# Performance work log

Measured on AMD Instinct MI355X. Metric: run time of the kernel, lower is better.

The kernel has to match this reference:

```python
import jax, jax.numpy as jnp
import numpy as np

N_NODES = 50000
N_EDGES = 300000
N_GRAPHS = 2048
N_FEATS = 128
DIM_OUT = 32


def setup_inputs() -> dict:
    key = jax.random.key(0)
    ks = jax.random.split(key, 10)
    def glorot(k, shape):
        fan_in, fan_out = shape
        lim = (6.0 / (fan_in + fan_out)) ** 0.5
        return jax.random.uniform(k, shape, jnp.float32, -lim, lim)
    x = jax.random.normal(ks[0], (N_NODES, N_FEATS), jnp.float32)
    edge_index = jax.random.randint(ks[1], (2, N_EDGES), 0, N_NODES, jnp.int64)
    batch = jnp.sort(jax.random.randint(ks[2], (N_NODES,), 0, N_GRAPHS, jnp.int64))
    return {
        "x": x,
        "edge_index": edge_index,
        "batch": batch,
        "W1": glorot(ks[3], (N_FEATS, 256)), "b1": jnp.zeros((256,), jnp.float32),
        "W2": glorot(ks[4], (256, 256)),     "b2": jnp.zeros((256,), jnp.float32),
        "W3": glorot(ks[5], (256, 256)),     "b3": jnp.zeros((256,), jnp.float32),
        "Wf1": glorot(ks[6], (256, 128)),    "bf1": jnp.zeros((128,), jnp.float32),
        "Wf2": glorot(ks[7], (128, DIM_OUT)), "bf2": jnp.zeros((DIM_OUT,), jnp.float32),
    }


def _gcn_norm(edge_index, num_nodes):
    # PyG GCNConv default: add self-loops, symmetric D^-1/2 (A+I) D^-1/2 norm.
    loop = jnp.arange(num_nodes, dtype=edge_index.dtype)
    src = jnp.concatenate([edge_index[0], loop])
    dst = jnp.concatenate([edge_index[1], loop])
    deg = jax.ops.segment_sum(jnp.ones_like(dst, jnp.float32), dst, num_segments=num_nodes)
    dinv = jnp.where(deg > 0, deg ** -0.5, 0.0)
    norm = dinv[src] * dinv[dst]  # [E + N]
    return src, dst, norm


def _gcn_conv(x, src, dst, norm, W, b):
    h = x @ W                                # [N, C] transform first (efficient)
    msg = h[src] * norm[:, None]             # gather + scale, [E+N, C]
    agg = jax.ops.segment_sum(msg, dst, num_segments=x.shape[0])
    return agg + b


def reference(x, edge_index, batch, W1, b1, W2, b2, W3, b3, Wf1, bf1, Wf2, bf2):
    n = x.shape[0]
    src, dst, norm = _gcn_norm(edge_index, n)
    h = jax.nn.relu(_gcn_conv(x, src, dst, norm, W1, b1))
    h = jax.nn.relu(_gcn_conv(h, src, dst, norm, W2, b2))
    h = jax.nn.relu(_gcn_conv(h, src, dst, norm, W3, b3))
    # global_mean_pool over batch segment ids
    sums = jax.ops.segment_sum(h, batch, num_segments=N_GRAPHS)
    cnts = jax.ops.segment_sum(jnp.ones((n,), jnp.float32), batch, num_segments=N_GRAPHS)
    hg = sums / jnp.maximum(cnts, 1.0)[:, None]
    h = jax.nn.relu(hg @ Wf1 + bf1)
    return h @ Wf2 + bf2  # [N_GRAPHS, DIM_OUT]
```

## Files before the change

kernel.cpp:

```cpp
#include <hip/hip_runtime.h>
#include <hip/hip_bf16.h>

#define NNODES 50000
#define NEDGES 300000
#define NGRAPH 2048
#define NFEAT  128
#define NHID   256
#define DOUT   32
#define NROWS  50048

typedef __bf16 bf16x8 __attribute__((ext_vector_type(8)));
typedef float  f32x4  __attribute__((ext_vector_type(4)));
typedef unsigned short ushort8v __attribute__((ext_vector_type(8)));
typedef __attribute__((address_space(1))) const void* gas_ptr;
typedef __attribute__((address_space(3))) void* las_ptr;

__device__ __forceinline__ float bf2f(unsigned short u) {
    return __uint_as_float(((unsigned)u) << 16);
}
__device__ __forceinline__ unsigned short f2bf(float f) {
    unsigned u = __float_as_uint(f);
    unsigned r = u + 0x7FFFu + ((u >> 16) & 1u);
    return (unsigned short)(r >> 16);
}


__global__ __launch_bounds__(256) void prep_k(const float* __restrict__ x, unsigned short* __restrict__ x16,
                                              const float* __restrict__ W1, const float* __restrict__ W2,
                                              const float* __restrict__ W3, const float* __restrict__ Wf1,
                                              const float* __restrict__ Wf2,
                                              unsigned short* __restrict__ Wt1, unsigned short* __restrict__ Wt2,
                                              unsigned short* __restrict__ Wt3, unsigned short* __restrict__ Wf1t,
                                              unsigned short* __restrict__ Wf2t,
                                              int* __restrict__ cnt, int* __restrict__ fill,
                                              int4* __restrict__ adj8z) {
    int idx = blockIdx.x * 256 + threadIdx.x;
    if (idx < 800000) {
        int i = idx * 8;
        float4 a = *(const float4*)&x[i];
        float4 b = *(const float4*)&x[i + 4];
        ushort8v o = { f2bf(a.x), f2bf(a.y), f2bf(a.z), f2bf(a.w),
                       f2bf(b.x), f2bf(b.y), f2bf(b.z), f2bf(b.w) };
        int row = idx >> 4, ch = idx & 15;
        ((ushort8v*)x16)[(size_t)(row << 4) | (ch ^ (row & 7))] = o;
        return;
    }
    int t = idx - 800000;
    if (t < 200704) {
        const float* W; unsigned short* Wt; int K, N, base; bool sw;
        if      (t <  32768) { W = W1;  Wt = Wt1;  K = 128; N = 256; base = 0;      sw = true; }
        else if (t <  98304) { W = W2;  Wt = Wt2;  K = 256; N = 256; base = 32768;  sw = true; }
        else if (t < 163840) { W = W3;  Wt = Wt3;  K = 256; N = 256; base = 98304;  sw = true; }
        else if (t < 196608) { W = Wf1; Wt = Wf1t; K = 256; N = 128; base = 163840; sw = false; }
        else                 { W = Wf2; Wt = Wf2t; K = 128; N = 32;  base = 196608; sw = false; }
        int i = t - base; int n = i / K, k = i - n * K;
        unsigned short v = f2bf(W[(size_t)k * N + n]);
        if (sw) Wt[(k >> 5) * 8192 + n * 32 + (k & 31)] = v;
        else    Wt[i] = v;
        return;
    }
    t -= 200704;
    if (t < NNODES) { cnt[t] = 0; fill[t] = 0; return; }
    t -= NNODES;
    if (t < 200000) { int4 z4 = {0, 0, 0, 0}; adj8z[t] = z4; }
}

__global__ __launch_bounds__(256) void edge_hist_k(const int* __restrict__ dst, int* cnt, int E) {
    int e = blockIdx.x * 256 + threadIdx.x;
    if (e < E) atomicAdd(&cnt[dst[e]], 1);
}

__global__ __launch_bounds__(1024) void scan_block_k(const int* __restrict__ cnt, int* __restrict__ rowp,
                                                     int* __restrict__ part, float* __restrict__ dinv,
                                                     int2* __restrict__ hdr, int n) {
    __shared__ int s[1024];
    int tid = threadIdx.x;
    int i = blockIdx.x * 1024 + tid;
    int v = (i < n) ? cnt[i] : 0;
    if (i < n) {
        float dv = rsqrtf((float)(v + 1));
        dinv[i] = dv;
        hdr[i] = make_int2(v, __float_as_int(dv * dv));
    }
    s[tid] = v;
    __syncthreads();
    for (int off = 1; off < 1024; off <<= 1) {
        int t = (tid >= off) ? s[tid - off] : 0;
        __syncthreads();
        s[tid] += t;
        __syncthreads();
    }
    if (i < n) rowp[i] = s[tid] - v;
    if (tid == 1023) part[blockIdx.x] = s[1023];
}

__global__ __launch_bounds__(256) void scatter_k(const int* __restrict__ src, const int* __restrict__ dst,
                                                 const int* __restrict__ rowp_pre, const int* __restrict__ part,
                                                 int* fill, const float* __restrict__ dinv,
                                                 int2* __restrict__ adj8, int2* __restrict__ adj,
                                                 int* __restrict__ rowp_fin,
                                                 const int* __restrict__ batch, int* __restrict__ gstart,
                                                 int E, int n, int nb) {
    __shared__ int s[64];
    int tid = threadIdx.x;
    if (tid < 64) s[tid] = (tid < nb) ? part[tid] : 0;
    __syncthreads();
    for (int off = 1; off < 64; off <<= 1) {
        int t = 0;
        if (tid < 64 && tid >= off) t = s[tid - off];
        __syncthreads();
        if (tid < 64) s[tid] += t;
        __syncthreads();
    }
    int gid = blockIdx.x * 256 + tid;
    if (gid <= n) {
        if (gid < n) {
            int ch = gid >> 10;
            int base = (ch == 0) ? 0 : s[ch - 1];
            rowp_fin[gid] = rowp_pre[gid] + base;
        } else {
            rowp_fin[n] = s[nb - 1];
        }
    }
    if (gid < n) {
        int b = batch[gid];
        int prev = (gid == 0) ? -1 : batch[gid - 1];
        for (int g = prev + 1; g <= b; ++g) gstart[g] = gid;
        if (gid == n - 1)
            for (int g = b + 1; g <= NGRAPH; ++g) gstart[g] = n;
    }
    if (gid < E) {
        int ss = src[gid], d = dst[gid];
        int f = atomicAdd(&fill[d], 1);
        int2 a; a.x = ss; a.y = __float_as_int(dinv[ss] * dinv[d]);
        if (f < 8) {
            adj8[d * 8 + f] = a;
        } else {
            int ch = d >> 10;
            int base = (ch == 0) ? 0 : s[ch - 1];
            adj[rowp_pre[d] + base + f] = a;
        }
    }
}

template<int CH>
__global__ __launch_bounds__(256) void agg_k(const unsigned short* __restrict__ T,
                                             const int4* __restrict__ adj8,
                                             const int2* __restrict__ hdr,
                                             const int* __restrict__ rowf,
                                             const int2* __restrict__ adj,
                                             unsigned short* __restrict__ z, int n) {
    int g  = threadIdx.x / CH;
    int li = threadIdx.x % CH;
    int node = blockIdx.x * (256 / CH) + g;
    if (node >= n) return;
    const ushort8v* tp = (const ushort8v*)T;
    int2 h = hdr[node];
    int deg = h.x;
    float sw = __int_as_float(h.y);
    ushort8v u = tp[(size_t)node * CH + (li ^ (node & 7))];
    int4 s4[4];
#pragma unroll
    for (int j = 0; j < 4; ++j) s4[j] = adj8[node * 4 + j];
    float ac[8];
#pragma unroll
    for (int k = 0; k < 8; ++k) ac[k] = bf2f(u[k]) * sw;
    int c[8]; float w[8];
#pragma unroll
    for (int j = 0; j < 4; ++j) {
        c[2 * j]     = s4[j].x; w[2 * j]     = __int_as_float(s4[j].y);
        c[2 * j + 1] = s4[j].z; w[2 * j + 1] = __int_as_float(s4[j].w);
    }
    ushort8v mm[8];
#pragma unroll
    for (int j = 0; j < 8; ++j) mm[j] = tp[(size_t)c[j] * CH + (li ^ (c[j] & 7))];
#pragma unroll
    for (int j = 0; j < 8; ++j)
#pragma unroll
        for (int k = 0; k < 8; ++k)
            ac[k] += bf2f(mm[j][k]) * w[j];
    if (deg > 8) {
        int e0 = rowf[node], e1 = e0 + deg;
        for (int e = e0 + 8; e < e1; e += 4) {
            int2 a2[4];
#pragma unroll
            for (int j = 0; j < 4; ++j) {
                int ee = e + j;
                a2[j] = (ee < e1) ? adj[ee] : make_int2(0, 0);
            }
            ushort8v m2[4];
#pragma unroll
            for (int j = 0; j < 4; ++j) m2[j] = tp[(size_t)a2[j].x * CH + (li ^ (a2[j].x & 7))];
#pragma unroll
            for (int j = 0; j < 4; ++j)
#pragma unroll
                for (int k = 0; k < 8; ++k)
                    ac[k] += bf2f(m2[j][k]) * __int_as_float(a2[j].y);
        }
    }
    ushort8v o;
#pragma unroll
    for (int k = 0; k < 8; ++k) o[k] = f2bf(ac[k]);
    ((ushort8v*)z)[(size_t)node * CH + (li ^ (node & 7))] = o;
}

template<int K>
__global__ __launch_bounds__(512, 2) void gemm_k(const unsigned short* __restrict__ A,
                                                 const unsigned short* __restrict__ Bsw,
                                                 const float* __restrict__ bias,
                                                 unsigned short* __restrict__ C,
                                                 int M, int flags, int ntiles) {
    constexpr int CPR = K / 8;
    constexpr int LP  = (64 * CPR) / 512;
    __shared__ unsigned short At[64 * K];
    __shared__ unsigned short Et[64 * 264];
    const int tid = threadIdx.x;
    const int lane = tid & 63;
    const int wave = tid >> 6;
    const int m = lane & 15, q = lane >> 4;
    const int wr = (wave >> 2) * 32;
    const int wc = (wave & 3) * 64;

    bf16x8 breg[K / 32][4];
#pragma unroll
    for (int kt = 0; kt < K / 32; ++kt)
#pragma unroll
        for (int j = 0; j < 4; ++j)
            breg[kt][j] = *(const bf16x8*)&Bsw[kt * 8192 + (wc + j * 16 + m) * 32 + q * 8];

    for (int t = blockIdx.x; t < ntiles; t += gridDim.x) {
        const size_t cbase = (size_t)t * 64 * CPR;
#pragma unroll
        for (int p = 0; p < LP; ++p) {
            int u = p * 512 + tid;
            __builtin_amdgcn_global_load_lds((gas_ptr)(A + (cbase + u) * 8),
                                             (las_ptr)&At[(p * 512 + wave * 64) * 8], 16, 0, 0);
        }
        __syncthreads();

        f32x4 acc[2][4] = {};
#pragma unroll
        for (int kt = 0; kt < K / 32; ++kt) {
            bf16x8 af[2];
#pragma unroll
            for (int i = 0; i < 2; ++i) {
                int lr = wr + i * 16 + m;
                af[i] = *(const bf16x8*)&At[(lr * CPR + ((kt * 4 + q) ^ (lr & 7))) * 8];
            }
#pragma unroll
            for (int i = 0; i < 2; ++i)
#pragma unroll
                for (int j = 0; j < 4; ++j)
                    acc[i][j] = __builtin_amdgcn_mfma_f32_16x16x32_bf16(af[i], breg[kt][j], acc[i][j], 0, 0, 0);
        }

#pragma unroll
        for (int i = 0; i < 2; ++i) {
#pragma unroll
            for (int j = 0; j < 4; ++j) {
                int c = wc + j * 16 + m;
                float bv = (flags & 2) ? bias[c] : 0.f;
#pragma unroll
                for (int r = 0; r < 4; ++r) {
                    float v = acc[i][j][r] + bv;
                    if (flags & 1) v = fmaxf(v, 0.f);
                    Et[(wr + i * 16 + q * 4 + r) * 264 + c] = f2bf(v);
                }
            }
        }
        __syncthreads();
#pragma unroll
        for (int u0 = 0; u0 < 4; ++u0) {
            int u = u0 * 512 + tid;
            int row = u >> 5, cc = u & 31;
            int rr = t * 64 + row;
            if (rr < M)
                ((ushort8v*)C)[(size_t)rr * 32 + (cc ^ (rr & 7))] = *(const ushort8v*)&Et[row * 264 + cc * 8];
        }
    }
}

__global__ __launch_bounds__(256) void pool_k(const unsigned short* __restrict__ h,
                                              const int* __restrict__ gstart,
                                              unsigned short* __restrict__ hg) {
    __shared__ float red[4][256];
    int g = blockIdx.x;
    int wave = threadIdx.x >> 6, lane = threadIdx.x & 63;
    int s = gstart[g], e = gstart[g + 1];
    int ch = lane >> 1, sub = lane & 1;
    const ushort4* hp = (const ushort4*)h;
    float4 acc = make_float4(0.f, 0.f, 0.f, 0.f);
    for (int i = s + wave; i < e; i += 4) {
        ushort4 v = hp[((size_t)i * 32 + (ch ^ (i & 7))) * 2 + sub];
        acc.x += bf2f(v.x); acc.y += bf2f(v.y); acc.z += bf2f(v.z); acc.w += bf2f(v.w);
    }
    *(float4*)&red[wave][lane * 4] = acc;
    __syncthreads();
    if (wave == 0) {
        float inv = 1.f / fmaxf((float)(e - s), 1.f);
        float v0 = red[0][lane*4+0] + red[1][lane*4+0] + red[2][lane*4+0] + red[3][lane*4+0];
        float v1 = red[0][lane*4+1] + red[1][lane*4+1] + red[2][lane*4+1] + red[3][lane*4+1];
        float v2 = red[0][lane*4+2] + red[1][lane*4+2] + red[2][lane*4+2] + red[3][lane*4+2];
        float v3 = red[0][lane*4+3] + red[1][lane*4+3] + red[2][lane*4+3] + red[3][lane*4+3];
        ushort4 o = { f2bf(v0 * inv), f2bf(v1 * inv), f2bf(v2 * inv), f2bf(v3 * inv) };
        ((ushort4*)(hg + (size_t)g * NHID))[lane] = o;
    }
}

__global__ __launch_bounds__(256) void mlp_head_k(const unsigned short* __restrict__ HG,
                                                  const unsigned short* __restrict__ Wf1t,
                                                  const unsigned short* __restrict__ Wf2t,
                                                  const float* __restrict__ bf1, const float* __restrict__ bf2,
                                                  float* __restrict__ out) {
    __shared__ unsigned short As1[128 * 32];
    __shared__ unsigned short Bs1[128 * 32];
    __shared__ unsigned short R[128 * 128];
    __shared__ unsigned short Bs2[32 * 128];
    const int tid = threadIdx.x;
    const int lane = tid & 63, wave = tid >> 6;
    const int m = lane & 15, q = lane >> 4;
    const int rowBase = blockIdx.x * 128;
    const int wr = (wave >> 1) * 64;
    const int wc = (wave & 1) * 64;

#pragma unroll
    for (int c2 = 0; c2 < 2; ++c2) {
        const unsigned short* g = &Wf2t[(c2 * 256 + tid) * 8];
        __builtin_amdgcn_global_load_lds((gas_ptr)g, (las_ptr)&Bs2[(c2 * 256 + wave * 64) * 8], 16, 0, 0);
    }

    f32x4 acc[4][4] = {};
    for (int kt = 0; kt < 256; kt += 32) {
#pragma unroll
        for (int c2 = 0; c2 < 2; ++c2) {
            int u = c2 * 256 + tid;
            int row = u >> 2, kp = u & 3;
            const unsigned short* ga = &HG[(size_t)(rowBase + row) * 256 + kt + kp * 8];
            const unsigned short* gb = &Wf1t[(size_t)row * 256 + kt + kp * 8];
            __builtin_amdgcn_global_load_lds((gas_ptr)ga, (las_ptr)&As1[(c2 * 256 + wave * 64) * 8], 16, 0, 0);
            __builtin_amdgcn_global_load_lds((gas_ptr)gb, (las_ptr)&Bs1[(c2 * 256 + wave * 64) * 8], 16, 0, 0);
        }
        __syncthreads();
        bf16x8 af[4], bfr[4];
#pragma unroll
        for (int i = 0; i < 4; ++i) af[i] = *(const bf16x8*)&As1[(wr + i * 16 + m) * 32 + q * 8];
#pragma unroll
        for (int j = 0; j < 4; ++j) bfr[j] = *(const bf16x8*)&Bs1[(wc + j * 16 + m) * 32 + q * 8];
#pragma unroll
        for (int i = 0; i < 4; ++i)
#pragma unroll
            for (int j = 0; j < 4; ++j)
                acc[i][j] = __builtin_amdgcn_mfma_f32_16x16x32_bf16(af[i], bfr[j], acc[i][j], 0, 0, 0);
        __syncthreads();
    }
#pragma unroll
    for (int i = 0; i < 4; ++i)
#pragma unroll
        for (int j = 0; j < 4; ++j) {
            int c = wc + j * 16 + m;
            float bv = bf1[c];
#pragma unroll
            for (int r = 0; r < 4; ++r) {
                int rr = wr + i * 16 + q * 4 + r;
                R[rr * 128 + c] = f2bf(fmaxf(acc[i][j][r] + bv, 0.f));
            }
        }
    __syncthreads();

    const int wr2 = wave * 32;
    f32x4 acc2[2][2] = {};
#pragma unroll
    for (int s2 = 0; s2 < 4; ++s2) {
        bf16x8 af2[2], bf22[2];
#pragma unroll
        for (int i = 0; i < 2; ++i) af2[i] = *(const bf16x8*)&R[(wr2 + i * 16 + m) * 128 + s2 * 32 + q * 8];
#pragma unroll
        for (int ct = 0; ct < 2; ++ct) bf22[ct] = *(const bf16x8*)&Bs2[(ct * 16 + m) * 128 + s2 * 32 + q * 8];
#pragma unroll
        for (int i = 0; i < 2; ++i)
#pragma unroll
            for (int ct = 0; ct < 2; ++ct)
                acc2[i][ct] = __builtin_amdgcn_mfma_f32_16x16x32_bf16(af2[i], bf22[ct], acc2[i][ct], 0, 0, 0);
    }
#pragma unroll
    for (int i = 0; i < 2; ++i)
#pragma unroll
        for (int ct = 0; ct < 2; ++ct) {
            int c = ct * 16 + m;
            float bv = bf2[c];
#pragma unroll
            for (int r = 0; r < 4; ++r) {
                int rr = rowBase + wr2 + i * 16 + q * 4 + r;
                out[(size_t)rr * 32 + c] = acc2[i][ct][r] + bv;
            }
        }
}

extern "C" void kernel_launch(void* const* d_in, const int* in_sizes, int n_in,
                              void* d_out, int out_size, void* d_ws, size_t ws_size,
                              hipStream_t stream) {
    const float* x    = (const float*)d_in[0];
    const int*   ei   = (const int*)d_in[1];
    const int*   batch= (const int*)d_in[2];
    const float* W1   = (const float*)d_in[3];
    const float* b1   = (const float*)d_in[4];
    const float* W2   = (const float*)d_in[5];
    const float* b2   = (const float*)d_in[6];
    const float* W3   = (const float*)d_in[7];
    const float* b3   = (const float*)d_in[8];
    const float* Wf1  = (const float*)d_in[9];
    const float* bf1  = (const float*)d_in[10];
    const float* Wf2  = (const float*)d_in[11];
    const float* bf2  = (const float*)d_in[12];
    float* out = (float*)d_out;

    const int* e_src = ei;
    const int* e_dst = ei + NEDGES;

    char* ws = (char*)d_ws;
    size_t off = 0;
    auto alloc = [&](size_t bytes) -> void* {
        void* p = (void*)(ws + off);
        off += (bytes + 255) & ~(size_t)255;
        return p;
    };
    unsigned short* X16 = (unsigned short*)alloc((size_t)NROWS * NFEAT * 2);
    unsigned short* Za  = (unsigned short*)alloc((size_t)NROWS * NFEAT * 2);
    unsigned short* Ha  = (unsigned short*)alloc((size_t)NROWS * NHID * 2);
    unsigned short* Zb  = (unsigned short*)alloc((size_t)NROWS * NHID * 2);
    unsigned short* Wt1 = (unsigned short*)alloc((size_t)NHID * NFEAT * 2);
    unsigned short* Wt2 = (unsigned short*)alloc((size_t)NHID * NHID * 2);
    unsigned short* Wt3 = (unsigned short*)alloc((size_t)NHID * NHID * 2);
    unsigned short* Wf1t= (unsigned short*)alloc((size_t)NFEAT * NHID * 2);
    unsigned short* Wf2t= (unsigned short*)alloc((size_t)DOUT * NFEAT * 2);
    unsigned short* HG  = (unsigned short*)alloc((size_t)NGRAPH * NHID * 2);
    float* dinv = (float*)alloc((size_t)NNODES * 4);
    int*   cnt  = (int*)alloc((size_t)NNODES * 4);
    int*   fill = (int*)alloc((size_t)NNODES * 4);
    int*   rowp = (int*)alloc((size_t)(NNODES + 1) * 4);
    int*   rowf = (int*)alloc((size_t)(NNODES + 1) * 4);
    int2*  adj8 = (int2*)alloc((size_t)NNODES * 8 * 8);
    int2*  adj  = (int2*)alloc((size_t)NEDGES * 8);
    int2*  hdr  = (int2*)alloc((size_t)NNODES * 8);
    int*   part = (int*)alloc((size_t)64 * 4);
    int*   gstart = (int*)alloc((size_t)(NGRAPH + 1) * 4);
    (void)alloc(131072);

    const int nb = (NNODES + 1023) / 1024;

    hipLaunchKernelGGL(prep_k, dim3((1250704 + 255) / 256), dim3(256), 0, stream,
                       x, X16, W1, W2, W3, Wf1, Wf2, Wt1, Wt2, Wt3, Wf1t, Wf2t, cnt, fill,
                       (int4*)adj8);
    hipLaunchKernelGGL(edge_hist_k, dim3((NEDGES + 255) / 256), dim3(256), 0, stream, e_dst, cnt, NEDGES);
    hipLaunchKernelGGL(scan_block_k, dim3(nb), dim3(1024), 0, stream, cnt, rowp, part, dinv, hdr, NNODES);
    hipLaunchKernelGGL(scatter_k, dim3((NEDGES + 255) / 256), dim3(256), 0, stream,
                       e_src, e_dst, rowp, part, fill, dinv, adj8, adj, rowf, batch, gstart,
                       NEDGES, NNODES, nb);

    const int ntiles = NROWS / 64;
    hipLaunchKernelGGL((agg_k<16>), dim3((NNODES + 15) / 16), dim3(256), 0, stream,
                       X16, (const int4*)adj8, hdr, rowf, adj, Za, NNODES);
    hipLaunchKernelGGL((gemm_k<128>), dim3(512), dim3(512), 0, stream,
                       Za, Wt1, b1, Ha, NNODES, 3, ntiles);
    hipLaunchKernelGGL((agg_k<32>), dim3((NNODES + 7) / 8), dim3(256), 0, stream,
                       Ha, (const int4*)adj8, hdr, rowf, adj, Zb, NNODES);
    hipLaunchKernelGGL((gemm_k<256>), dim3(512), dim3(512), 0, stream,
                       Zb, Wt2, b2, Ha, NNODES, 3, ntiles);
    hipLaunchKernelGGL((agg_k<32>), dim3((NNODES + 7) / 8), dim3(256), 0, stream,
                       Ha, (const int4*)adj8, hdr, rowf, adj, Zb, NNODES);
    hipLaunchKernelGGL((gemm_k<256>), dim3(512), dim3(512), 0, stream,
                       Zb, Wt3, b3, Ha, NNODES, 3, ntiles);

    hipLaunchKernelGGL(pool_k, dim3(NGRAPH), dim3(256), 0, stream, Ha, gstart, HG);

    hipLaunchKernelGGL(mlp_head_k, dim3(NGRAPH / 128), dim3(256), 0, stream,
                       HG, Wf1t, Wf2t, bf1, bf2, out);
}
```

Before: 280.2 us.

## Quantize hidden activations to int8 with per-row scales for aggregation gathers

The first two GEMMs now emit int8 activations with a per-row absmax scale instead of bf16. A new aggregation kernel gathers these int8 rows, dequantizes with the row scales and accumulates in fp32. The aim is to halve the bytes moved by the bandwidth-bound neighbor gathers. It adds quantization error beyond bf16 and extra epilogue work for the reduction and packing.

```diff
diff --git a/kernel.cpp b/kernel.cpp
--- a/kernel.cpp
+++ b/kernel.cpp
@@ -22,6 +22,9 @@
     unsigned u = __float_as_uint(f);
     unsigned r = u + 0x7FFFu + ((u >> 16) & 1u);
     return (unsigned short)(r >> 16);
+}
+__device__ __forceinline__ float sb2f(unsigned v, int k) {
+    return (float)((signed char)(v >> (8 * k)));
 }
 
 
@@ -204,11 +207,86 @@
     ((ushort8v*)z)[(size_t)node * CH + (li ^ (node & 7))] = o;
 }
 
-template<int K>
+__global__ __launch_bounds__(256) void agg_q_k(const unsigned char* __restrict__ Hq,
+                                               const float* __restrict__ csc,
+                                               const int4* __restrict__ adj8,
+                                               const int2* __restrict__ hdr,
+                                               const int* __restrict__ rowf,
+                                               const int2* __restrict__ adj,
+                                               unsigned short* __restrict__ z, int n) {
+    int g  = threadIdx.x >> 5;
+    int li = threadIdx.x & 31;
+    int node = blockIdx.x * 8 + g;
+    if (node >= n) return;
+    const uint2* qp = (const uint2*)Hq;
+    int2 h = hdr[node];
+    int deg = h.x;
+    float swgt = __int_as_float(h.y) * csc[node];
+    uint2 u = qp[(size_t)node * 32 + li];
+    int4 s4[4];
+#pragma unroll
+    for (int j = 0; j < 4; ++j) s4[j] = adj8[node * 4 + j];
+    int c[8]; float w[8];
+#pragma unroll
+    for (int j = 0; j < 4; ++j) {
+        c[2 * j]     = s4[j].x; w[2 * j]     = __int_as_float(s4[j].y);
+        c[2 * j + 1] = s4[j].z; w[2 * j + 1] = __int_as_float(s4[j].w);
+    }
+    uint2 mm[8];
+#pragma unroll
+    for (int j = 0; j < 8; ++j) mm[j] = qp[(size_t)c[j] * 32 + li];
+    float ws[8];
+#pragma unroll
+    for (int j = 0; j < 8; ++j) ws[j] = w[j] * csc[c[j]];
+    float ac[8];
+#pragma unroll
+    for (int k = 0; k < 4; ++k) {
+        ac[k]     = sb2f(u.x, k) * swgt;
+        ac[k + 4] = sb2f(u.y, k) * swgt;
+    }
+#pragma unroll
+    for (int j = 0; j < 8; ++j)
+#pragma unroll
+        for (int k = 0; k < 4; ++k) {
+            ac[k]     += sb2f(mm[j].x, k) * ws[j];
+            ac[k + 4] += sb2f(mm[j].y, k) * ws[j];
+        }
+    if (deg > 8) {
+        int e0 = rowf[node], e1 = e0 + deg;
+        for (int e = e0 + 8; e < e1; e += 4) {
+            int2 a2[4];
+#pragma unroll
+            for (int j = 0; j < 4; ++j) {
+                int ee = e + j;
+                a2[j] = (ee < e1) ? adj[ee] : make_int2(0, 0);
+            }
+            uint2 m2[4]; float w2[4];
+#pragma unroll
+            for (int j = 0; j < 4; ++j) m2[j] = qp[(size_t)a2[j].x * 32 + li];
+#pragma unroll
+            for (int j = 0; j < 4; ++j) w2[j] = __int_as_float(a2[j].y) * csc[a2[j].x];
+#pragma unroll
+            for (int j = 0; j < 4; ++j)
+#pragma unroll
+                for (int k = 0; k < 4; ++k) {
+                    ac[k]     += sb2f(m2[j].x, k) * w2[j];
+                    ac[k + 4] += sb2f(m2[j].y, k) * w2[j];
+                }
+        }
+    }
+    ushort8v o;
+#pragma unroll
+    for (int k = 0; k < 8; ++k) o[k] = f2bf(ac[k]);
+    ((ushort8v*)z)[(size_t)node * 32 + (li ^ (node & 7))] = o;
+}
+
+template<int K, bool QOUT>
 __global__ __launch_bounds__(512, 2) void gemm_k(const unsigned short* __restrict__ A,
                                                  const unsigned short* __restrict__ Bsw,
                                                  const float* __restrict__ bias,
                                                  unsigned short* __restrict__ C,
+                                                 unsigned char* __restrict__ Cq,
+                                                 float* __restrict__ csc,
                                                  int M, int flags, int ntiles) {
     constexpr int CPR = K / 8;
     constexpr int LP  = (64 * CPR) / 512;
@@ -269,13 +347,51 @@
             }
         }
         __syncthreads();
-#pragma unroll
-        for (int u0 = 0; u0 < 4; ++u0) {
-            int u = u0 * 512 + tid;
-            int row = u >> 5, cc = u & 31;
+
+        if (QOUT) {
+            int row = tid >> 3, ch8 = tid & 7;
             int rr = t * 64 + row;
-            if (rr < M)
-                ((ushort8v*)C)[(size_t)rr * 32 + (cc ^ (rr & 7))] = *(const ushort8v*)&Et[row * 264 + cc * 8];
+            ushort8v e[4];
+#pragma unroll
+            for (int k2 = 0; k2 < 4; ++k2)
+                e[k2] = *(const ushort8v*)&Et[row * 264 + ch8 * 32 + k2 * 8];
+            float mx = 0.f;
+#pragma unroll
+            for (int k2 = 0; k2 < 4; ++k2)
+#pragma unroll
+                for (int k = 0; k < 8; ++k) mx = fmaxf(mx, fabsf(bf2f(e[k2][k])));
+            mx = fmaxf(mx, __shfl_xor(mx, 1, 64));
+            mx = fmaxf(mx, __shfl_xor(mx, 2, 64));
+            mx = fmaxf(mx, __shfl_xor(mx, 4, 64));
+            float inv = (mx > 0.f) ? 127.f / mx : 0.f;
+            unsigned pk[8];
+#pragma unroll
+            for (int w2 = 0; w2 < 8; ++w2) {
+                unsigned p = 0;
+#pragma unroll
+                for (int b = 0; b < 4; ++b) {
+                    int e8 = w2 * 4 + b;
+                    float v = bf2f(e[e8 >> 3][e8 & 7]);
+                    int qv = (int)rintf(v * inv);
+                    p |= ((unsigned)(qv & 255)) << (8 * b);
+                }
+                pk[w2] = p;
+            }
+            if (rr < M) {
+                uint4* dst = (uint4*)&Cq[(size_t)rr * 256 + ch8 * 32];
+                dst[0] = make_uint4(pk[0], pk[1], pk[2], pk[3]);
+                dst[1] = make_uint4(pk[4], pk[5], pk[6], pk[7]);
+                if (ch8 == 0) csc[rr] = mx * (1.f / 127.f);
+            }
+        } else {
+#pragma unroll
+            for (int u0 = 0; u0 < 4; ++u0) {
+                int u = u0 * 512 + tid;
+                int row = u >> 5, cc = u & 31;
+                int rr = t * 64 + row;
+                if (rr < M)
+                    ((ushort8v*)C)[(size_t)rr * 32 + (cc ^ (rr & 7))] = *(const ushort8v*)&Et[row * 264 + cc * 8];
+            }
         }
     }
 }
@@ -426,8 +542,10 @@
     };
     unsigned short* X16 = (unsigned short*)alloc((size_t)NROWS * NFEAT * 2);
     unsigned short* Za  = (unsigned short*)alloc((size_t)NROWS * NFEAT * 2);
+    unsigned short* Zb  = (unsigned short*)alloc((size_t)NROWS * NHID * 2);
     unsigned short* Ha  = (unsigned short*)alloc((size_t)NROWS * NHID * 2);
-    unsigned short* Zb  = (unsigned short*)alloc((size_t)NROWS * NHID * 2);
+    unsigned char*  Hq  = (unsigned char*)alloc((size_t)NROWS * NHID);
+    float*          csc = (float*)alloc((size_t)NROWS * 4);
     unsigned short* Wt1 = (unsigned short*)alloc((size_t)NHID * NFEAT * 2);
     unsigned short* Wt2 = (unsigned short*)alloc((size_t)NHID * NHID * 2);
     unsigned short* Wt3 = (unsigned short*)alloc((size_t)NHID * NHID * 2);
@@ -460,16 +578,16 @@
     const int ntiles = NROWS / 64;
     hipLaunchKernelGGL((agg_k<16>), dim3((NNODES + 15) / 16), dim3(256), 0, stream,
                        X16, (const int4*)adj8, hdr, rowf, adj, Za, NNODES);
-    hipLaunchKernelGGL((gemm_k<128>), dim3(512), dim3(512), 0, stream,
-                       Za, Wt1, b1, Ha, NNODES, 3, ntiles);
-    hipLaunchKernelGGL((agg_k<32>), dim3((NNODES + 7) / 8), dim3(256), 0, stream,
-                       Ha, (const int4*)adj8, hdr, rowf, adj, Zb, NNODES);
-    hipLaunchKernelGGL((gemm_k<256>), dim3(512), dim3(512), 0, stream,
-                       Zb, Wt2, b2, Ha, NNODES, 3, ntiles);
-    hipLaunchKernelGGL((agg_k<32>), dim3((NNODES + 7) / 8), dim3(256), 0, stream,
-                       Ha, (const int4*)adj8, hdr, rowf, adj, Zb, NNODES);
-    hipLaunchKernelGGL((gemm_k<256>), dim3(512), dim3(512), 0, stream,
-                       Zb, Wt3, b3, Ha, NNODES, 3, ntiles);
+    hipLaunchKernelGGL((gemm_k<128, true>), dim3(512), dim3(512), 0, stream,
+                       Za, Wt1, b1, (unsigned short*)nullptr, Hq, csc, NNODES, 3, ntiles);
+    hipLaunchKernelGGL(agg_q_k, dim3((NNODES + 7) / 8), dim3(256), 0, stream,
+                       Hq, csc, (const int4*)adj8, hdr, rowf, adj, Zb, NNODES);
+    hipLaunchKernelGGL((gemm_k<256, true>), dim3(512), dim3(512), 0, stream,
+                       Zb, Wt2, b2, (unsigned short*)nullptr, Hq, csc, NNODES, 3, ntiles);
+    hipLaunchKernelGGL(agg_q_k, dim3((NNODES + 7) / 8), dim3(256), 0, stream,
+                       Hq, csc, (const int4*)adj8, hdr, rowf, adj, Zb, NNODES);
+    hipLaunchKernelGGL((gemm_k<256, false>), dim3(512), dim3(512), 0, stream,
+                       Zb, Wt3, b3, Ha, Hq, csc, NNODES, 3, ntiles);
 
     hipLaunchKernelGGL(pool_k, dim3(NGRAPH), dim3(256), 0, stream, Ha, gstart, HG);
 
```

Measured after the change: 268.3 us. -4.2%, faster.
